# Performance work log

Hardware: AMD Instinct MI355X
Metric: run time of the kernel (lower is better)

## Reference

```python
import jax, jax.numpy as jnp
import numpy as np
import math

B, N, C = 8, 1024, 256
NUM_HEAD = 4
HEAD_DIM = C // NUM_HEAD
K_NN = 5
SAMPLE_RATIO = 0.25
CLUSTER_NUM = max(math.ceil(N * SAMPLE_RATIO), 1)
EPS = 1e-6


def cluster_dpc_knn(x, cluster_num, k):
    # DPC-KNN clustering (faithful to TCFormer's cluster_dpc_knn, run under no_grad in torch)
    b, n, c = x.shape
    sq = jnp.sum(x * x, axis=-1)
    d2 = sq[:, :, None] + sq[:, None, :] - 2.0 * jnp.einsum('bic,bjc->bij', x, x)
    dist = jnp.sqrt(jnp.maximum(d2, 0.0)) / jnp.sqrt(jnp.asarray(c, x.dtype))  # (b,n,n)
    # k smallest distances per token (includes self, dist 0)
    neg_near, _ = jax.lax.top_k(-dist, k)
    dist_nearest = -neg_near
    density = jnp.exp(-jnp.mean(dist_nearest ** 2, axis=-1))  # (b,n)
    # deterministic tiny noise for tie-breaking (torch adds rand*1e-6)
    density = density + jax.random.uniform(jax.random.key(42), density.shape, dtype=density.dtype) * 1e-6
    mask = (density[:, None, :] > density[:, :, None]).astype(x.dtype)
    dist_max = jnp.max(dist.reshape(b, -1), axis=-1)[:, None, None]
    d_ind = jnp.min(dist * mask + dist_max * (1.0 - mask), axis=-1)  # distance indicator
    score = d_ind * density
    _, index_down = jax.lax.top_k(score, cluster_num)  # (b,cluster_num) cluster centers
    dist_c = jnp.take_along_axis(dist, index_down[:, :, None], axis=1)  # (b,cn,n)
    idx_cluster = jnp.argmin(dist_c, axis=1)  # (b,n)
    # ensure each center maps to its own cluster id
    bidx = jnp.arange(b)[:, None]
    idx_cluster = idx_cluster.at[bidx, index_down].set(jnp.broadcast_to(jnp.arange(cluster_num)[None, :], (b, cluster_num)))
    return idx_cluster


def setup_inputs() -> dict:
    key = jax.random.key(0)
    ks = jax.random.split(key, 6)
    w_scale = 1.0 / jnp.sqrt(jnp.asarray(C, jnp.float32))
    x_token = jax.random.normal(ks[0], (B, N, C), dtype=jnp.float32)
    Wq = jax.random.normal(ks[1], (C, C), dtype=jnp.float32) * w_scale
    Wk = jax.random.normal(ks[2], (C, C), dtype=jnp.float32) * w_scale
    Wv = jax.random.normal(ks[3], (C, C), dtype=jnp.float32) * w_scale
    Wp = jax.random.normal(ks[4], (C, C), dtype=jnp.float32) * w_scale
    bp = jax.random.normal(ks[5], (C,), dtype=jnp.float32) * 0.01
    return {"x_token": x_token, "Wq": Wq, "Wk": Wk, "Wv": Wv, "Wp": Wp, "bp": bp}


def reference(x_token, Wq, Wk, Wv, Wp, bp):
    b, n, c = x_token.shape
    scale = HEAD_DIM ** -0.5
    idx_cluster = cluster_dpc_knn(x_token, CLUSTER_NUM, K_NN)  # (b,n) int
    q = (x_token @ Wq.T).reshape(b, n, NUM_HEAD, HEAD_DIM).transpose(0, 2, 1, 3)
    k = (x_token @ Wk.T).reshape(b, n, NUM_HEAD, HEAD_DIM).transpose(0, 2, 1, 3)
    v = (x_token @ Wv.T).reshape(b, n, NUM_HEAD, HEAD_DIM).transpose(0, 2, 1, 3)
    scores = jnp.einsum('bhid,bhjd->bhij', q, k) * scale  # (b,h,n,n)
    # scatter into (b,cluster_num,n,c) + sum over clusters == mask scores by same-cluster
    same = (idx_cluster[:, :, None] == idx_cluster[:, None, :])[:, None, :, :]
    attn = jnp.where(same, scores, 0.0)
    # original: masked_fill(attn == 0, -1e9) then exp in float32
    attn = jnp.where(attn == 0.0, -1e9, attn)
    attn = jnp.exp(attn.astype(jnp.float32))
    attn = (attn + EPS / n) / (jnp.sum(attn, axis=-1, keepdims=True) + EPS)
    out = jnp.einsum('bhij,bhjd->bhid', attn, v).transpose(0, 2, 1, 3).reshape(b, n, c)
    return out @ Wp.T + bp
```

## Files before the change

### kernel.cpp

```cpp
#include <hip/hip_runtime.h>
#include <math.h>

#define B_ 8
#define N_ 1024
#define C_ 256
#define H_ 4
#define D_ 64
#define CN_ 256
#define EPS_ 1e-6f

__device__ __forceinline__ unsigned rotl32(unsigned x, int r){ return (x<<r)|(x>>(32-r)); }

__device__ float tf_noise(unsigned gid){
  unsigned c0 = (gid >= 4096u) ? gid - 4096u : gid;
  unsigned c1 = c0 + 4096u;
  const unsigned k0 = 0u, k1 = 42u;
  const unsigned ks2 = k0 ^ k1 ^ 0x1BD11BDAu;
  unsigned x0 = c0 + k0, x1 = c1 + k1;
  const int R0[4] = {13,15,26,6};
  const int R1[4] = {17,29,16,24};
  #pragma unroll
  for (int i=0;i<4;i++){ x0 += x1; x1 = rotl32(x1,R0[i]); x1 ^= x0; }
  x0 += k1; x1 += ks2 + 1u;
  #pragma unroll
  for (int i=0;i<4;i++){ x0 += x1; x1 = rotl32(x1,R1[i]); x1 ^= x0; }
  x0 += ks2; x1 += k0 + 2u;
  #pragma unroll
  for (int i=0;i<4;i++){ x0 += x1; x1 = rotl32(x1,R0[i]); x1 ^= x0; }
  x0 += k0; x1 += k1 + 3u;
  #pragma unroll
  for (int i=0;i<4;i++){ x0 += x1; x1 = rotl32(x1,R1[i]); x1 ^= x0; }
  x0 += k1; x1 += ks2 + 4u;
  #pragma unroll
  for (int i=0;i<4;i++){ x0 += x1; x1 = rotl32(x1,R0[i]); x1 ^= x0; }
  x0 += ks2; x1 += k0 + 5u;
  unsigned bits = (gid >= 4096u) ? x1 : x0;
  return __uint_as_float(0x3F800000u | (bits >> 9)) - 1.0f;
}

__global__ __launch_bounds__(256) void k_sq(const float* __restrict__ x, float* __restrict__ sq){
  int row = blockIdx.x * 4 + (threadIdx.x >> 6);
  int l = threadIdx.x & 63;
  const float* p = x + (size_t)row * C_;
  float s = 0.f;
  #pragma unroll
  for (int t=0;t<4;t++){ float v = p[l + 64*t]; s += v*v; }
  #pragma unroll
  for (int m=32;m;m>>=1) s += __shfl_xor(s, m);
  if (l==0) sq[row] = s;
}

__global__ __launch_bounds__(256) void k_dist(const float* __restrict__ x, const float* __restrict__ sq,
                                              float* __restrict__ dist){
  int b = blockIdx.z;
  int bi = blockIdx.y, bj = blockIdx.x;
  const float* xb = x + (size_t)b * N_ * C_;
  __shared__ __align__(16) float As[32][68];
  __shared__ __align__(16) float Bs[32][68];
  int tid = threadIdx.x;
  int tx = tid & 15, ty = tid >> 4;
  int lrow = tid >> 3, lk = (tid & 7)*4;
  float acc[4][4] = {};
  for (int k0=0;k0<C_;k0+=32){
    #pragma unroll
    for (int rr=0;rr<2;rr++){
      int r = rr*32 + lrow;
      float4 a = *(const float4*)(xb + (size_t)(bi*64 + r)*C_ + k0 + lk);
      As[lk+0][r]=a.x; As[lk+1][r]=a.y; As[lk+2][r]=a.z; As[lk+3][r]=a.w;
      float4 c = *(const float4*)(xb + (size_t)(bj*64 + r)*C_ + k0 + lk);
      Bs[lk+0][r]=c.x; Bs[lk+1][r]=c.y; Bs[lk+2][r]=c.z; Bs[lk+3][r]=c.w;
    }
    __syncthreads();
    #pragma unroll
    for (int kk=0;kk<32;kk++){
      float4 av = *(const float4*)&As[kk][ty*4];
      float4 bv = *(const float4*)&Bs[kk][tx*4];
      float a4[4] = {av.x,av.y,av.z,av.w};
      float b4[4] = {bv.x,bv.y,bv.z,bv.w};
      #pragma unroll
      for (int r=0;r<4;r++)
        #pragma unroll
        for (int c2=0;c2<4;c2++) acc[r][c2] += a4[r]*b4[c2];
    }
    __syncthreads();
  }
  float* dbase = dist + (size_t)b * N_ * N_;
  #pragma unroll
  for (int r=0;r<4;r++){
    int i = bi*64 + ty*4 + r;
    float si = sq[b*N_ + i];
    #pragma unroll
    for (int c2=0;c2<4;c2++){
      int j = bj*64 + tx*4 + c2;
      float d2 = si + sq[b*N_ + j] - 2.f*acc[r][c2];
      dbase[(size_t)i*N_ + j] = sqrtf(fmaxf(d2, 0.f)) * 0.0625f;
    }
  }
}

__global__ __launch_bounds__(256) void k_top5(const float* __restrict__ dist, float* __restrict__ density,
                                              float* __restrict__ rowmax){
  int row = blockIdx.x * 4 + (threadIdx.x >> 6);
  int l = threadIdx.x & 63;
  const float* p = dist + (size_t)row * N_;
  float t[5] = {1e30f,1e30f,1e30f,1e30f,1e30f};
  float mx = 0.f;
  #pragma unroll
  for (int q2=0;q2<16;q2++){
    float v = p[l + 64*q2];
    mx = fmaxf(mx, v);
    if (v < t[4]){
      t[4] = v;
      #pragma unroll
      for (int a=4;a>0;a--) if (t[a] < t[a-1]) { float tmp=t[a]; t[a]=t[a-1]; t[a-1]=tmp; }
    }
  }
  #pragma unroll
  for (int m=32;m;m>>=1) mx = fmaxf(mx, __shfl_xor(mx, m));
  float sumsq = 0.f;
  int hi = 0;
  #pragma unroll
  for (int a=0;a<5;a++){
    float head = (hi==0)?t[0]:(hi==1)?t[1]:(hi==2)?t[2]:(hi==3)?t[3]:(hi==4)?t[4]:1e30f;
    float m = head;
    #pragma unroll
    for (int mm=32;mm;mm>>=1) m = fminf(m, __shfl_xor(m, mm));
    sumsq += m*m;
    unsigned long long ball = __ballot(head == m);
    if (l == (__ffsll(ball) - 1)) hi++;
  }
  if (l == 0){
    float msq = sumsq / 5.0f;
    density[row] = expf(-msq) + tf_noise((unsigned)row) * 1e-6f;
    rowmax[row] = mx;
  }
}

__global__ __launch_bounds__(256) void k_bmax(const float* __restrict__ rowmax, float* __restrict__ bmax){
  int b = blockIdx.x; int t = threadIdx.x;
  float m = fmaxf(fmaxf(rowmax[b*N_+t], rowmax[b*N_+t+256]),
                  fmaxf(rowmax[b*N_+t+512], rowmax[b*N_+t+768]));
  __shared__ float s[256];
  s[t]=m; __syncthreads();
  for (int d=128; d; d>>=1){ if (t<d) s[t]=fmaxf(s[t],s[t+d]); __syncthreads(); }
  if (t==0) bmax[b]=s[0];
}

__global__ __launch_bounds__(256) void k_dind(const float* __restrict__ dist, const float* __restrict__ density,
                                              const float* __restrict__ bmax, float* __restrict__ score){
  int row = blockIdx.x * 4 + (threadIdx.x >> 6);
  int b = row >> 10;
  int l = threadIdx.x & 63;
  const float* p = dist + (size_t)row * N_;
  const float* db = density + b*N_;
  float di = density[row];
  float m = bmax[b];
  #pragma unroll
  for (int q2=0;q2<16;q2++){
    int j = l + 64*q2;
    float dj = db[j];
    if (dj > di) m = fminf(m, p[j]);
  }
  #pragma unroll
  for (int mm=32;mm;mm>>=1) m = fminf(m, __shfl_xor(m, mm));
  if (l==0) score[row] = m * di;
}

__global__ __launch_bounds__(1024) void k_top256(const float* __restrict__ score, int* __restrict__ idxdown){
  int b = blockIdx.x; int t = threadIdx.x;
  __shared__ float sv[1024];
  __shared__ int si[1024];
  sv[t] = score[b*N_ + t]; si[t] = t;
  __syncthreads();
  for (int k = 2; k <= 1024; k <<= 1){
    for (int j = k >> 1; j > 0; j >>= 1){
      int l = t ^ j;
      if (l > t){
        bool up = ((t & k) == 0);
        float a = sv[t], b2 = sv[l]; int ai = si[t], bi2 = si[l];
        bool prec = (a > b2) || (a == b2 && ai < bi2);
        bool dosw = up ? (!prec) : prec;
        if (dosw){ sv[t]=b2; sv[l]=a; si[t]=bi2; si[l]=ai; }
      }
      __syncthreads();
    }
  }
  if (t < CN_) idxdown[b*CN_ + t] = si[t];
}

__global__ __launch_bounds__(256) void k_assign(const float* __restrict__ dist, const int* __restrict__ idxdown,
                                                int* __restrict__ idxclu){
  int b = blockIdx.y;
  int j = blockIdx.x*256 + threadIdx.x;
  __shared__ int cen[256];
  cen[threadIdx.x] = idxdown[b*CN_ + threadIdx.x];
  __syncthreads();
  const float* dbase = dist + (size_t)b*N_*N_;
  float best = 1e30f; int bk = 0;
  for (int k=0;k<CN_;k++){
    float d = dbase[(size_t)cen[k]*N_ + j];
    if (d < best){ best = d; bk = k; }
  }
  idxclu[b*N_ + j] = bk;
}

__global__ void k_setcenters(const int* __restrict__ idxdown, int* __restrict__ idxclu){
  int b = blockIdx.x; int t = threadIdx.x;
  idxclu[b*N_ + idxdown[b*CN_ + t]] = t;
}

__global__ void k_zero(int* p, int n){ int i = blockIdx.x*256+threadIdx.x; if (i<n) p[i]=0; }

__global__ void k_hist(const int* __restrict__ idxclu, int* __restrict__ cnt){
  int i = blockIdx.x*256 + threadIdx.x;
  int b = i >> 10;
  atomicAdd(&cnt[b*CN_ + idxclu[i]], 1);
}

__global__ __launch_bounds__(256) void k_scan(const int* __restrict__ cnt, int* __restrict__ off,
                                              int* __restrict__ cur){
  int b = blockIdx.x; int t = threadIdx.x;
  __shared__ int s[256];
  int mine = cnt[b*CN_ + t];
  s[t] = mine;
  __syncthreads();
  for (int d = 1; d < 256; d <<= 1){
    int v = 0;
    if (t >= d) v = s[t - d];
    __syncthreads();
    if (t >= d) s[t] += v;
    __syncthreads();
  }
  int excl = s[t] - mine;
  off[b*CN_ + t] = excl;
  cur[b*CN_ + t] = excl;
}

__global__ void k_scatter(const int* __restrict__ idxclu, int* __restrict__ cur, int* __restrict__ members){
  int i = blockIdx.x*256 + threadIdx.x;
  int b = i >> 10; int tok = i & 1023;
  int c = idxclu[i];
  int p = atomicAdd(&cur[b*CN_ + c], 1);
  members[b*N_ + p] = tok;
}

__global__ __launch_bounds__(256) void k_gemm_nt(const float* __restrict__ X, const float* __restrict__ W,
                                                 const float* __restrict__ bias, float* __restrict__ Y){
  __shared__ __align__(16) float As[32][68];
  __shared__ __align__(16) float Bs[32][68];
  int bx = blockIdx.x;
  int by = blockIdx.y;
  int tid = threadIdx.x;
  int tx = tid & 15, ty = tid >> 4;
  int lrow = tid >> 3, lk = (tid & 7)*4;
  float acc[4][4] = {};
  for (int k0=0;k0<256;k0+=32){
    #pragma unroll
    for (int rr=0;rr<2;rr++){
      int r = rr*32 + lrow;
      float4 a = *(const float4*)(X + (size_t)(by*64 + r)*256 + k0 + lk);
      As[lk+0][r]=a.x; As[lk+1][r]=a.y; As[lk+2][r]=a.z; As[lk+3][r]=a.w;
      float4 c = *(const float4*)(W + (size_t)(bx*64 + r)*256 + k0 + lk);
      Bs[lk+0][r]=c.x; Bs[lk+1][r]=c.y; Bs[lk+2][r]=c.z; Bs[lk+3][r]=c.w;
    }
    __syncthreads();
    #pragma unroll
    for (int kk=0;kk<32;kk++){
      float4 av = *(const float4*)&As[kk][ty*4];
      float4 bv = *(const float4*)&Bs[kk][tx*4];
      float a4[4] = {av.x,av.y,av.z,av.w};
      float b4[4] = {bv.x,bv.y,bv.z,bv.w};
      #pragma unroll
      for (int r=0;r<4;r++)
        #pragma unroll
        for (int c2=0;c2<4;c2++) acc[r][c2] += a4[r]*b4[c2];
    }
    __syncthreads();
  }
  #pragma unroll
  for (int r=0;r<4;r++){
    int m = by*64 + ty*4 + r;
    #pragma unroll
    for (int c2=0;c2<4;c2++){
      int o = bx*64 + tx*4 + c2;
      float v = acc[r][c2];
      if (bias) v += bias[o];
      Y[(size_t)m*256 + o] = v;
    }
  }
}

__global__ void k_vsum(const float* __restrict__ v, float* __restrict__ vsum){
  int b = blockIdx.x; int c = threadIdx.x;
  float s = 0.f;
  for (int i=0;i<N_;i++) s += v[((size_t)b*N_ + i)*C_ + c];
  vsum[b*C_ + c] = s;
}

__global__ __launch_bounds__(256) void k_attn(const float* __restrict__ q, const float* __restrict__ kmat,
                                              const float* __restrict__ v, const float* __restrict__ vsum,
                                              const int* __restrict__ idxclu, const int* __restrict__ off,
                                              const int* __restrict__ cnt, const int* __restrict__ members,
                                              float* __restrict__ att){
  int bi = blockIdx.x;
  int b = bi >> 10;
  int h = threadIdx.x >> 6, l = threadIdx.x & 63;
  int c = idxclu[bi];
  int o = off[b*CN_ + c], m = cnt[b*CN_ + c];
  int ch = h*64 + l;
  float qv = q[(size_t)bi*C_ + ch];
  float acc = 0.f, den = 0.f;
  const int* mem = members + b*N_ + o;
  for (int t=0;t<m;t++){
    int j = mem[t];
    size_t base = ((size_t)(b*N_ + j))*C_ + ch;
    float p = qv * kmat[base];
    #pragma unroll
    for (int mm=32;mm;mm>>=1) p += __shfl_xor(p, mm);
    float s = p * 0.125f;
    float e = (s == 0.0f) ? 0.0f : expf(s);
    den += e;
    acc += e * v[base];
  }
  float outv = (acc + (EPS_/1024.0f) * vsum[b*C_ + ch]) / (den + EPS_);
  att[(size_t)bi*C_ + ch] = outv;
}

extern "C" void kernel_launch(void* const* d_in, const int* in_sizes, int n_in,
                              void* d_out, int out_size, void* d_ws, size_t ws_size,
                              hipStream_t stream){
  const float* x  = (const float*)d_in[0];
  const float* Wq = (const float*)d_in[1];
  const float* Wk = (const float*)d_in[2];
  const float* Wv = (const float*)d_in[3];
  const float* Wp = (const float*)d_in[4];
  const float* bp = (const float*)d_in[5];
  float* out = (float*)d_out;

  float* ws = (float*)d_ws;
  float* dist    = ws;
  float* q       = dist + (size_t)B_*N_*N_;
  float* kk      = q    + (size_t)B_*N_*C_;
  float* v       = kk   + (size_t)B_*N_*C_;
  float* att     = v    + (size_t)B_*N_*C_;
  float* sq      = att  + (size_t)B_*N_*C_;
  float* rowmax  = sq + B_*N_;
  float* bmax    = rowmax + B_*N_;
  float* density = bmax + 16;
  float* score   = density + B_*N_;
  float* vsum    = score + B_*N_;
  int* idxdown   = (int*)(vsum + B_*C_);
  int* idxclu    = idxdown + B_*CN_;
  int* cnt       = idxclu + B_*N_;
  int* cur       = cnt + B_*CN_;
  int* off       = cur + B_*CN_;
  int* members   = off + B_*CN_;

  k_zero<<<16,256,0,stream>>>(cnt, 4096);
  k_sq<<<B_*N_/4,256,0,stream>>>(x, sq);
  k_dist<<<dim3(16,16,8),256,0,stream>>>(x, sq, dist);
  k_top5<<<B_*N_/4,256,0,stream>>>(dist, density, rowmax);
  k_bmax<<<8,256,0,stream>>>(rowmax, bmax);
  k_dind<<<B_*N_/4,256,0,stream>>>(dist, density, bmax, score);
  k_top256<<<8,1024,0,stream>>>(score, idxdown);
  k_assign<<<dim3(4,8),256,0,stream>>>(dist, idxdown, idxclu);
  k_setcenters<<<8,256,0,stream>>>(idxdown, idxclu);
  k_hist<<<32,256,0,stream>>>(idxclu, cnt);
  k_scan<<<8,256,0,stream>>>(cnt, off, cur);
  k_scatter<<<32,256,0,stream>>>(idxclu, cur, members);
  k_gemm_nt<<<dim3(4,128),256,0,stream>>>(x, Wq, nullptr, q);
  k_gemm_nt<<<dim3(4,128),256,0,stream>>>(x, Wk, nullptr, kk);
  k_gemm_nt<<<dim3(4,128),256,0,stream>>>(x, Wv, nullptr, v);
  k_vsum<<<8,256,0,stream>>>(v, vsum);
  k_attn<<<B_*N_,256,0,stream>>>(q, kk, v, vsum, idxclu, off, cnt, members, att);
  k_gemm_nt<<<dim3(4,128),256,0,stream>>>(att, Wp, bp, out);
}
```

Baseline: 365.1 us.

## Use 128x128 register-tiled GEMMs, batch QKV projections, fuse cluster build, split vsum

Replaces the 64x64 SGEMM tiles (4x4 per thread) in the distance and projection kernels with 128x128 tiles (8x8 per thread), register-staged global loads and float4 stores. The three QKV projections become one launch using blockIdx.z. Histogram, scan and scatter are merged into a single per-batch kernel using shared-memory atomics, which removes the zeroing kernel. The serial column sum of V is split into a two-stage parallel reduction. The aim is more reuse per shared-memory load and fewer launches. The cost is higher register pressure and fewer blocks, which lowers occupancy.

```diff
diff --git a/kernel.cpp b/kernel.cpp
--- a/kernel.cpp
+++ b/kernel.cpp
@@ -50,51 +50,123 @@
   if (l==0) sq[row] = s;
 }
 
-__global__ __launch_bounds__(256) void k_dist(const float* __restrict__ x, const float* __restrict__ sq,
-                                              float* __restrict__ dist){
-  int b = blockIdx.z;
-  int bi = blockIdx.y, bj = blockIdx.x;
+__global__ __launch_bounds__(256) void k_dist2(const float* __restrict__ x, const float* __restrict__ sq,
+                                               float* __restrict__ dist){
+  int b = blockIdx.z, bi = blockIdx.y, bj = blockIdx.x;
   const float* xb = x + (size_t)b * N_ * C_;
-  __shared__ __align__(16) float As[32][68];
-  __shared__ __align__(16) float Bs[32][68];
+  __shared__ float As[16][132];
+  __shared__ float Bs[16][132];
   int tid = threadIdx.x;
   int tx = tid & 15, ty = tid >> 4;
-  int lrow = tid >> 3, lk = (tid & 7)*4;
-  float acc[4][4] = {};
-  for (int k0=0;k0<C_;k0+=32){
-    #pragma unroll
-    for (int rr=0;rr<2;rr++){
-      int r = rr*32 + lrow;
-      float4 a = *(const float4*)(xb + (size_t)(bi*64 + r)*C_ + k0 + lk);
-      As[lk+0][r]=a.x; As[lk+1][r]=a.y; As[lk+2][r]=a.z; As[lk+3][r]=a.w;
-      float4 c = *(const float4*)(xb + (size_t)(bj*64 + r)*C_ + k0 + lk);
-      Bs[lk+0][r]=c.x; Bs[lk+1][r]=c.y; Bs[lk+2][r]=c.z; Bs[lk+3][r]=c.w;
-    }
-    __syncthreads();
-    #pragma unroll
-    for (int kk=0;kk<32;kk++){
-      float4 av = *(const float4*)&As[kk][ty*4];
-      float4 bv = *(const float4*)&Bs[kk][tx*4];
-      float a4[4] = {av.x,av.y,av.z,av.w};
-      float b4[4] = {bv.x,bv.y,bv.z,bv.w};
+  float acc[8][8] = {};
+  for (int k0=0;k0<C_;k0+=16){
+    float4 ra[2], rb[2];
+    #pragma unroll
+    for (int f=0;f<2;f++){
+      int idx = tid*2+f;
+      int row = idx>>2, kq = idx&3;
+      ra[f] = *(const float4*)(xb + (size_t)(bi*128+row)*C_ + k0 + kq*4);
+      rb[f] = *(const float4*)(xb + (size_t)(bj*128+row)*C_ + k0 + kq*4);
+    }
+    __syncthreads();
+    #pragma unroll
+    for (int f=0;f<2;f++){
+      int idx = tid*2+f;
+      int row = idx>>2, kq = idx&3;
+      As[kq*4+0][row]=ra[f].x; As[kq*4+1][row]=ra[f].y; As[kq*4+2][row]=ra[f].z; As[kq*4+3][row]=ra[f].w;
+      Bs[kq*4+0][row]=rb[f].x; Bs[kq*4+1][row]=rb[f].y; Bs[kq*4+2][row]=rb[f].z; Bs[kq*4+3][row]=rb[f].w;
+    }
+    __syncthreads();
+    #pragma unroll
+    for (int kk=0;kk<16;kk++){
+      float4 a0 = *(const float4*)&As[kk][ty*8];
+      float4 a1 = *(const float4*)&As[kk][ty*8+4];
+      float4 b0 = *(const float4*)&Bs[kk][tx*8];
+      float4 b1 = *(const float4*)&Bs[kk][tx*8+4];
+      float av[8]={a0.x,a0.y,a0.z,a0.w,a1.x,a1.y,a1.z,a1.w};
+      float bv[8]={b0.x,b0.y,b0.z,b0.w,b1.x,b1.y,b1.z,b1.w};
       #pragma unroll
-      for (int r=0;r<4;r++)
+      for (int r=0;r<8;r++)
         #pragma unroll
-        for (int c2=0;c2<4;c2++) acc[r][c2] += a4[r]*b4[c2];
-    }
-    __syncthreads();
-  }
+        for (int c=0;c<8;c++) acc[r][c] += av[r]*bv[c];
+    }
+  }
+  int ibase = bi*128 + ty*8, jbase = bj*128 + tx*8;
+  float sj[8];
+  #pragma unroll
+  for (int c=0;c<8;c++) sj[c] = sq[b*N_ + jbase + c];
   float* dbase = dist + (size_t)b * N_ * N_;
   #pragma unroll
-  for (int r=0;r<4;r++){
-    int i = bi*64 + ty*4 + r;
+  for (int r=0;r<8;r++){
+    int i = ibase + r;
     float si = sq[b*N_ + i];
-    #pragma unroll
-    for (int c2=0;c2<4;c2++){
-      int j = bj*64 + tx*4 + c2;
-      float d2 = si + sq[b*N_ + j] - 2.f*acc[r][c2];
-      dbase[(size_t)i*N_ + j] = sqrtf(fmaxf(d2, 0.f)) * 0.0625f;
-    }
+    float o[8];
+    #pragma unroll
+    for (int c=0;c<8;c++){
+      float d2 = si + sj[c] - 2.f*acc[r][c];
+      o[c] = sqrtf(fmaxf(d2, 0.f)) * 0.0625f;
+    }
+    *(float4*)(dbase + (size_t)i*N_ + jbase)     = make_float4(o[0],o[1],o[2],o[3]);
+    *(float4*)(dbase + (size_t)i*N_ + jbase + 4) = make_float4(o[4],o[5],o[6],o[7]);
+  }
+}
+
+__global__ __launch_bounds__(256) void k_gemm2(const float* __restrict__ X,
+    const float* __restrict__ W0, const float* __restrict__ W1, const float* __restrict__ W2,
+    const float* __restrict__ bias,
+    float* __restrict__ Y0, float* __restrict__ Y1, float* __restrict__ Y2){
+  const float* W = (blockIdx.z==0)?W0:(blockIdx.z==1)?W1:W2;
+  float* Y = (blockIdx.z==0)?Y0:(blockIdx.z==1)?Y1:Y2;
+  int bi = blockIdx.y, bj = blockIdx.x;
+  __shared__ float As[16][132];
+  __shared__ float Bs[16][132];
+  int tid = threadIdx.x;
+  int tx = tid & 15, ty = tid >> 4;
+  float acc[8][8] = {};
+  for (int k0=0;k0<C_;k0+=16){
+    float4 ra[2], rb[2];
+    #pragma unroll
+    for (int f=0;f<2;f++){
+      int idx = tid*2+f;
+      int row = idx>>2, kq = idx&3;
+      ra[f] = *(const float4*)(X + (size_t)(bi*128+row)*C_ + k0 + kq*4);
+      rb[f] = *(const float4*)(W + (size_t)(bj*128+row)*C_ + k0 + kq*4);
+    }
+    __syncthreads();
+    #pragma unroll
+    for (int f=0;f<2;f++){
+      int idx = tid*2+f;
+      int row = idx>>2, kq = idx&3;
+      As[kq*4+0][row]=ra[f].x; As[kq*4+1][row]=ra[f].y; As[kq*4+2][row]=ra[f].z; As[kq*4+3][row]=ra[f].w;
+      Bs[kq*4+0][row]=rb[f].x; Bs[kq*4+1][row]=rb[f].y; Bs[kq*4+2][row]=rb[f].z; Bs[kq*4+3][row]=rb[f].w;
+    }
+    __syncthreads();
+    #pragma unroll
+    for (int kk=0;kk<16;kk++){
+      float4 a0 = *(const float4*)&As[kk][ty*8];
+      float4 a1 = *(const float4*)&As[kk][ty*8+4];
+      float4 b0 = *(const float4*)&Bs[kk][tx*8];
+      float4 b1 = *(const float4*)&Bs[kk][tx*8+4];
+      float av[8]={a0.x,a0.y,a0.z,a0.w,a1.x,a1.y,a1.z,a1.w};
+      float bv[8]={b0.x,b0.y,b0.z,b0.w,b1.x,b1.y,b1.z,b1.w};
+      #pragma unroll
+      for (int r=0;r<8;r++)
+        #pragma unroll
+        for (int c=0;c<8;c++) acc[r][c] += av[r]*bv[c];
+    }
+  }
+  int jbase = bj*128 + tx*8;
+  float bs[8];
+  #pragma unroll
+  for (int c=0;c<8;c++) bs[c] = bias ? bias[jbase+c] : 0.f;
+  #pragma unroll
+  for (int r=0;r<8;r++){
+    int m = bi*128 + ty*8 + r;
+    float o[8];
+    #pragma unroll
+    for (int c=0;c<8;c++) o[c] = acc[r][c] + bs[c];
+    *(float4*)(Y + (size_t)m*C_ + jbase)     = make_float4(o[0],o[1],o[2],o[3]);
+    *(float4*)(Y + (size_t)m*C_ + jbase + 4) = make_float4(o[4],o[5],o[6],o[7]);
   }
 }
 
@@ -209,91 +281,57 @@
   idxclu[b*N_ + idxdown[b*CN_ + t]] = t;
 }
 
-__global__ void k_zero(int* p, int n){ int i = blockIdx.x*256+threadIdx.x; if (i<n) p[i]=0; }
-
-__global__ void k_hist(const int* __restrict__ idxclu, int* __restrict__ cnt){
-  int i = blockIdx.x*256 + threadIdx.x;
-  int b = i >> 10;
-  atomicAdd(&cnt[b*CN_ + idxclu[i]], 1);
-}
-
-__global__ __launch_bounds__(256) void k_scan(const int* __restrict__ cnt, int* __restrict__ off,
-                                              int* __restrict__ cur){
+__global__ __launch_bounds__(256) void k_build(const int* __restrict__ idxclu, int* __restrict__ off,
+                                               int* __restrict__ cnt, int* __restrict__ members){
   int b = blockIdx.x; int t = threadIdx.x;
-  __shared__ int s[256];
-  int mine = cnt[b*CN_ + t];
-  s[t] = mine;
-  __syncthreads();
-  for (int d = 1; d < 256; d <<= 1){
-    int v = 0;
-    if (t >= d) v = s[t - d];
-    __syncthreads();
-    if (t >= d) s[t] += v;
-    __syncthreads();
-  }
-  int excl = s[t] - mine;
-  off[b*CN_ + t] = excl;
-  cur[b*CN_ + t] = excl;
-}
-
-__global__ void k_scatter(const int* __restrict__ idxclu, int* __restrict__ cur, int* __restrict__ members){
-  int i = blockIdx.x*256 + threadIdx.x;
-  int b = i >> 10; int tok = i & 1023;
-  int c = idxclu[i];
-  int p = atomicAdd(&cur[b*CN_ + c], 1);
-  members[b*N_ + p] = tok;
-}
-
-__global__ __launch_bounds__(256) void k_gemm_nt(const float* __restrict__ X, const float* __restrict__ W,
-                                                 const float* __restrict__ bias, float* __restrict__ Y){
-  __shared__ __align__(16) float As[32][68];
-  __shared__ __align__(16) float Bs[32][68];
-  int bx = blockIdx.x;
-  int by = blockIdx.y;
-  int tid = threadIdx.x;
-  int tx = tid & 15, ty = tid >> 4;
-  int lrow = tid >> 3, lk = (tid & 7)*4;
-  float acc[4][4] = {};
-  for (int k0=0;k0<256;k0+=32){
-    #pragma unroll
-    for (int rr=0;rr<2;rr++){
-      int r = rr*32 + lrow;
-      float4 a = *(const float4*)(X + (size_t)(by*64 + r)*256 + k0 + lk);
-      As[lk+0][r]=a.x; As[lk+1][r]=a.y; As[lk+2][r]=a.z; As[lk+3][r]=a.w;
-      float4 c = *(const float4*)(W + (size_t)(bx*64 + r)*256 + k0 + lk);
-      Bs[lk+0][r]=c.x; Bs[lk+1][r]=c.y; Bs[lk+2][r]=c.z; Bs[lk+3][r]=c.w;
-    }
-    __syncthreads();
-    #pragma unroll
-    for (int kk=0;kk<32;kk++){
-      float4 av = *(const float4*)&As[kk][ty*4];
-      float4 bv = *(const float4*)&Bs[kk][tx*4];
-      float a4[4] = {av.x,av.y,av.z,av.w};
-      float b4[4] = {bv.x,bv.y,bv.z,bv.w};
-      #pragma unroll
-      for (int r=0;r<4;r++)
-        #pragma unroll
-        for (int c2=0;c2<4;c2++) acc[r][c2] += a4[r]*b4[c2];
-    }
-    __syncthreads();
-  }
-  #pragma unroll
-  for (int r=0;r<4;r++){
-    int m = by*64 + ty*4 + r;
-    #pragma unroll
-    for (int c2=0;c2<4;c2++){
-      int o = bx*64 + tx*4 + c2;
-      float v = acc[r][c2];
-      if (bias) v += bias[o];
-      Y[(size_t)m*256 + o] = v;
-    }
-  }
-}
-
-__global__ void k_vsum(const float* __restrict__ v, float* __restrict__ vsum){
+  __shared__ int sc[256], so[256];
+  sc[t] = 0;
+  __syncthreads();
+  int cl[4];
+  #pragma unroll
+  for (int i=0;i<4;i++){
+    cl[i] = idxclu[b*N_ + i*256 + t];
+    atomicAdd(&sc[cl[i]], 1);
+  }
+  __syncthreads();
+  int mine = sc[t];
+  so[t] = mine;
+  __syncthreads();
+  for (int d=1; d<256; d<<=1){
+    int v2 = 0;
+    if (t>=d) v2 = so[t-d];
+    __syncthreads();
+    if (t>=d) so[t] += v2;
+    __syncthreads();
+  }
+  int excl = so[t] - mine;
+  off[b*CN_+t] = excl;
+  cnt[b*CN_+t] = mine;
+  sc[t] = excl;
+  __syncthreads();
+  #pragma unroll
+  for (int i=0;i<4;i++){
+    int p = atomicAdd(&sc[cl[i]], 1);
+    members[b*N_ + p] = i*256 + t;
+  }
+}
+
+__global__ __launch_bounds__(256) void k_vsum1(const float* __restrict__ v, float* __restrict__ vsp){
+  int p = blockIdx.x;
+  int b = p >> 4, s = p & 15;
+  int c = threadIdx.x;
+  float acc = 0.f;
+  const float* base = v + ((size_t)b*N_ + s*64)*C_ + c;
+  #pragma unroll 8
+  for (int i=0;i<64;i++) acc += base[(size_t)i*C_];
+  vsp[(size_t)p*C_ + c] = acc;
+}
+
+__global__ __launch_bounds__(256) void k_vsum2(const float* __restrict__ vsp, float* __restrict__ vsum){
   int b = blockIdx.x; int c = threadIdx.x;
   float s = 0.f;
-  for (int i=0;i<N_;i++) s += v[((size_t)b*N_ + i)*C_ + c];
+  #pragma unroll
+  for (int i=0;i<16;i++) s += vsp[((size_t)b*16 + i)*C_ + c];
   vsum[b*C_ + c] = s;
 }
 
@@ -343,35 +381,31 @@
   float* kk      = q    + (size_t)B_*N_*C_;
   float* v       = kk   + (size_t)B_*N_*C_;
   float* att     = v    + (size_t)B_*N_*C_;
-  float* sq      = att  + (size_t)B_*N_*C_;
+  float* vsp     = att  + (size_t)B_*N_*C_;
+  float* vsum    = vsp + 128*C_;
+  float* sq      = vsum + B_*C_;
   float* rowmax  = sq + B_*N_;
   float* bmax    = rowmax + B_*N_;
   float* density = bmax + 16;
   float* score   = density + B_*N_;
-  float* vsum    = score + B_*N_;
-  int* idxdown   = (int*)(vsum + B_*C_);
+  int* idxdown   = (int*)(score + B_*N_);
   int* idxclu    = idxdown + B_*CN_;
   int* cnt       = idxclu + B_*N_;
-  int* cur       = cnt + B_*CN_;
-  int* off       = cur + B_*CN_;
+  int* off       = cnt + B_*CN_;
   int* members   = off + B_*CN_;
 
-  k_zero<<<16,256,0,stream>>>(cnt, 4096);
   k_sq<<<B_*N_/4,256,0,stream>>>(x, sq);
-  k_dist<<<dim3(16,16,8),256,0,stream>>>(x, sq, dist);
+  k_dist2<<<dim3(8,8,8),256,0,stream>>>(x, sq, dist);
   k_top5<<<B_*N_/4,256,0,stream>>>(dist, density, rowmax);
   k_bmax<<<8,256,0,stream>>>(rowmax, bmax);
   k_dind<<<B_*N_/4,256,0,stream>>>(dist, density, bmax, score);
   k_top256<<<8,1024,0,stream>>>(score, idxdown);
   k_assign<<<dim3(4,8),256,0,stream>>>(dist, idxdown, idxclu);
   k_setcenters<<<8,256,0,stream>>>(idxdown, idxclu);
-  k_hist<<<32,256,0,stream>>>(idxclu, cnt);
-  k_scan<<<8,256,0,stream>>>(cnt, off, cur);
-  k_scatter<<<32,256,0,stream>>>(idxclu, cur, members);
-  k_gemm_nt<<<dim3(4,128),256,0,stream>>>(x, Wq, nullptr, q);
-  k_gemm_nt<<<dim3(4,128),256,0,stream>>>(x, Wk, nullptr, kk);
-  k_gemm_nt<<<dim3(4,128),256,0,stream>>>(x, Wv, nullptr, v);
-  k_vsum<<<8,256,0,stream>>>(v, vsum);
+  k_build<<<8,256,0,stream>>>(idxclu, off, cnt, members);
+  k_gemm2<<<dim3(2,64,3),256,0,stream>>>(x, Wq, Wk, Wv, nullptr, q, kk, v);
+  k_vsum1<<<128,256,0,stream>>>(v, vsp);
+  k_vsum2<<<8,256,0,stream>>>(vsp, vsum);
   k_attn<<<B_*N_,256,0,stream>>>(q, kk, v, vsum, idxclu, off, cnt, members, att);
-  k_gemm_nt<<<dim3(4,128),256,0,stream>>>(att, Wp, bp, out);
-}
+  k_gemm2<<<dim3(2,64,1),256,0,stream>>>(att, Wp, Wp, Wp, bp, out, out, out);
+}
```

After: 337.5 us. -7.6%, faster.
